# Kernel tuning notes

Measured on AMD Instinct MI355X. Metric: run time of the kernel, lower is better.

The kernel has to match this reference:

```python
import jax, jax.numpy as jnp
import numpy as np

E = 1024   # embed_dim
H = 16     # num_heads
D = E // H # head_dim
BS = 512   # block_size
G = 128    # global_len
B = 1
S = 8192


def setup_inputs() -> dict:
    key = jax.random.key(0)
    ks = jax.random.split(key, 7)
    w_scale = 0.02
    return {
        "token_hidden_states": jax.random.normal(ks[0], (B, S, E), jnp.float32),
        "global_hidden_states": jax.random.normal(ks[1], (B, G, E), jnp.float32),
        "attention_mask": jnp.zeros((B, S), jnp.float32),  # additive float mask
        "Wq": jax.random.normal(ks[2], (E, E), jnp.float32) * w_scale,
        "Wk": jax.random.normal(ks[3], (E, E), jnp.float32) * w_scale,
        "Wv": jax.random.normal(ks[4], (E, E), jnp.float32) * w_scale,
        "Wo": jax.random.normal(ks[5], (E, E), jnp.float32) * w_scale,
    }


def _shape(x):
    # [B, L, E] -> [B, H, L, D]
    b, l, _ = x.shape
    return x.reshape(b, l, H, D).transpose(0, 2, 1, 3)


def reference(token_hidden_states, global_hidden_states, attention_mask, Wq, Wk, Wv, Wo):
    b, s, _ = token_hidden_states.shape
    g = global_hidden_states.shape[1]
    n = s // BS  # num_blocks
    scaling = D ** -0.5

    local_q = _shape(token_hidden_states @ Wq * scaling)
    local_k = _shape(token_hidden_states @ Wk)
    local_v = _shape(token_hidden_states @ Wv)
    global_q = _shape(global_hidden_states @ Wq * scaling)
    global_k = _shape(global_hidden_states @ Wk)
    global_v = _shape(global_hidden_states @ Wv)

    # ---- global attention: global queries attend to [global + all local] keys
    k_cat = jnp.concatenate([global_k, local_k], axis=2)   # [B,H,G+S,D]
    v_cat = jnp.concatenate([global_v, local_v], axis=2)
    ext_mask = jnp.pad(attention_mask, ((0, 0), (g, 0)))    # [B,G+S]
    gw = jnp.einsum('bhgf,bhxf->bhgx', global_q, k_cat) + ext_mask[:, None, None, :]
    gp = jax.nn.softmax(gw, axis=-1)
    g_out = jnp.einsum('bhgx,bhxf->bhgf', gp, v_cat)        # [B,H,G,D]
    g_out = g_out.transpose(0, 2, 1, 3).reshape(b, g, E) @ Wo

    # ---- local attention: block-local + global keys
    bq = local_q.reshape(b, H, n, BS, D)
    bk = local_k.reshape(b, H, n, BS, D)
    bv = local_v.reshape(b, H, n, BS, D)
    ext_mask_l = jnp.pad(attention_mask.reshape(b, n, BS), ((0, 0), (0, 0), (g, 0)))  # [B,N,G+K]
    l2g = jnp.einsum('bhnkf,bhgf->bhnkg', bq, global_k)     # [B,H,N,K,G]
    l2l = jnp.einsum('bhnkf,bhnxf->bhnkx', bq, bk)          # [B,H,N,K,K]
    lw = jnp.concatenate([l2g, l2l], axis=-1) + ext_mask_l[:, None, :, None, :]
    lp = jax.nn.softmax(lw, axis=-1)
    l_out = (jnp.einsum('bhnkg,bhgf->bhnkf', lp[..., :g], global_v)
             + jnp.einsum('bhnkx,bhnxf->bhnkf', lp[..., g:], bv))  # [B,H,N,K,D]
    l_out = l_out.transpose(0, 2, 3, 1, 4).reshape(b, s, E) @ Wo

    return (l_out, g_out)
```

## Files before the change

kernel.cpp:

```cpp
#include <hip/hip_runtime.h>
#include <stdint.h>

#define S_LEN  8192
#define G_LEN  128
#define E_DIM  1024
#define H_NUM  16
#define BS_LEN 512
#define R_TOT  8320
#define KBLK   128
#define XBLK   1040
#define NSPL   10
#define SPLW   832

typedef _Float16 half8    __attribute__((ext_vector_type(8)));
typedef _Float16 half4    __attribute__((ext_vector_type(4)));
typedef float    floatx4  __attribute__((ext_vector_type(4)));
typedef float    floatx16 __attribute__((ext_vector_type(16)));

#define QSCALE 0.18033688011112042f

#define OFF_XP   0
#define OFF_AOP  0
#define OFF_WP   17039360
#define SZ_WP1   2097152
#define OFF_QP   25427968
#define OFF_KP   42467328
#define OFF_VP   59506688
#define OFF_FH   76546048
#define OFF_OG   76579328
#define OFF_LG   81822208

__device__ __forceinline__ floatx16 zero16() {
  floatx16 v;
#pragma unroll
  for (int i = 0; i < 16; ++i) v[i] = 0.0f;
  return v;
}
__device__ __forceinline__ floatx4 zero4() {
  floatx4 v;
#pragma unroll
  for (int i = 0; i < 4; ++i) v[i] = 0.0f;
  return v;
}

__device__ __forceinline__ void gl_lds16(const void* g, void* l) {
  __builtin_amdgcn_global_load_lds(
      (const __attribute__((address_space(1))) void*)g,
      (__attribute__((address_space(3))) void*)l, 16, 0, 0);
}

__device__ __forceinline__ int pk_f16x2(float a, float b) {
  return __builtin_bit_cast(int, __builtin_amdgcn_cvt_pkrtz(a, b));
}

__global__ __launch_bounds__(256) void prep_k(const float* __restrict__ tok,
                                              const float* __restrict__ glob,
                                              const float* __restrict__ Wq,
                                              const float* __restrict__ Wk,
                                              const float* __restrict__ Wv,
                                              const float* __restrict__ Wo,
                                              const float* __restrict__ mask,
                                              char* __restrict__ ws) {
  __shared__ __align__(16) _Float16 tile[64 * 132];
  const int bx  = blockIdx.x;
  const int tid = threadIdx.x;
  if (bx < 1040) {
    const int r0 = (bx >> 3) * 64;
    const int c0 = (bx & 7) * 128;
#pragma unroll
    for (int kk = 0; kk < 8; ++kk) {
      int f   = tid + kk * 256;
      int row = f >> 5;
      int c4  = (f & 31) * 4;
      int r   = r0 + row;
      const float* src = (r < G_LEN) ? glob + (size_t)r * E_DIM
                                     : tok + (size_t)(r - G_LEN) * E_DIM;
      float4 v = *(const float4*)&src[c0 + c4];
      half4 h;
      h[0] = (_Float16)v.x; h[1] = (_Float16)v.y; h[2] = (_Float16)v.z; h[3] = (_Float16)v.w;
      *(half4*)&tile[row * 132 + c4] = h;
    }
    __syncthreads();
    _Float16* Xp = (_Float16*)(ws + OFF_XP);
#pragma unroll
    for (int uu = 0; uu < 4; ++uu) {
      int u    = tid + uu * 256;
      int kb_l = u >> 6;
      int row  = u & 63;
      half4 a = *(const half4*)&tile[row * 132 + kb_l * 8];
      half4 b = *(const half4*)&tile[row * 132 + kb_l * 8 + 4];
      half8 o;
      o[0] = a[0]; o[1] = a[1]; o[2] = a[2]; o[3] = a[3];
      o[4] = b[0]; o[5] = b[1]; o[6] = b[2]; o[7] = b[3];
      int kb = (c0 >> 3) + kb_l;
      *(half8*)&Xp[((size_t)kb * R_TOT + r0 + row) * 8] = o;
    }
  } else {
    int t = (bx - 1040) * 256 + tid;
    const int NW = 4 * KBLK * 1024;
    if (t < NW) {
      int w   = t >> 17;
      int rem = t & 131071;
      int kb  = rem >> 10;
      int n   = rem & 1023;
      const float* W = (w == 0) ? Wq : (w == 1) ? Wk : (w == 2) ? Wv : Wo;
      half8 v;
#pragma unroll
      for (int j = 0; j < 8; ++j)
        v[j] = (_Float16)W[(size_t)(kb * 8 + j) * 1024 + n];
      *(half8*)(ws + OFF_WP + (size_t)w * SZ_WP1 + (size_t)(kb * 1024 + n) * 16) = v;
    } else {
      int t2 = t - NW;
      if (t2 < R_TOT) {
        _Float16* fh = (_Float16*)(ws + OFF_FH);
        float m = (t2 < G_LEN) ? 0.0f : mask[t2 - G_LEN];
        fh[t2] = (_Float16)__expf(m);
      }
    }
  }
}

__device__ __forceinline__ void gemm_tile(const _Float16* __restrict__ Ap,
                                          const _Float16* __restrict__ Bp,
                                          int m0, int n0, _Float16* lds,
                                          floatx4 acc[4][4]) {
  const int tid  = threadIdx.x;
  const int wave = tid >> 6;
  const int lane = tid & 63;
  const int quad = lane >> 4;
  const int l16  = lane & 15;
  _Float16* As = lds;
  _Float16* Bs = lds + 8 * 128 * 8;
  const int wm = (wave >> 1) * 64;
  const int wn = (wave & 1) * 64;
  for (int step = 0; step < 16; ++step) {
#pragma unroll
    for (int ui = 0; ui < 8; ++ui) {
      const int u   = wave * 8 + ui;
      const int isB = u >> 4;
      const int vv  = u & 15;
      const int kb  = vv >> 1;
      const int rh  = vv & 1;
      const _Float16* src =
          isB ? Bp + (size_t)((step * 8 + kb) * 1024 + n0 + rh * 64 + lane) * 8
              : Ap + (size_t)((step * 8 + kb) * R_TOT + m0 + rh * 64 + lane) * 8;
      _Float16* dst = (isB ? Bs : As) + (kb * 128 + rh * 64) * 8;
      gl_lds16(src, dst);
    }
    __syncthreads();
#pragma unroll
    for (int kk = 0; kk < 2; ++kk) {
      half8 af[4], bf[4];
#pragma unroll
      for (int mt = 0; mt < 4; ++mt)
        af[mt] = *(const half8*)(As + ((kk * 4 + quad) * 128 + wm + mt * 16 + l16) * 8);
#pragma unroll
      for (int nt = 0; nt < 4; ++nt)
        bf[nt] = *(const half8*)(Bs + ((kk * 4 + quad) * 128 + wn + nt * 16 + l16) * 8);
#pragma unroll
      for (int mt = 0; mt < 4; ++mt)
#pragma unroll
        for (int nt = 0; nt < 4; ++nt)
          acc[mt][nt] = __builtin_amdgcn_mfma_f32_16x16x32_f16(bf[nt], af[mt], acc[mt][nt], 0, 0, 0);
    }
    __syncthreads();
  }
}

__global__ __launch_bounds__(256) void qkv_gemm_k(char* __restrict__ ws) {
  __shared__ __align__(16) _Float16 lds[2 * 8 * 128 * 8];
  const int z  = blockIdx.x >> 3;
  const int n0 = (blockIdx.x & 7) * 128;
  const int m0 = blockIdx.y * 128;
  floatx4 acc[4][4];
#pragma unroll
  for (int a = 0; a < 4; ++a)
#pragma unroll
    for (int b = 0; b < 4; ++b) acc[a][b] = zero4();
  gemm_tile((const _Float16*)(ws + OFF_XP),
            (const _Float16*)(ws + OFF_WP + (size_t)z * SZ_WP1), m0, n0, lds, acc);

  const int lane = threadIdx.x & 63, wave = threadIdx.x >> 6;
  const int quad = lane >> 4, l16 = lane & 15;
  const int wm = (wave >> 1) * 64, wn = (wave & 1) * 64;
  if (z < 2) {
    _Float16* dst = (_Float16*)(ws + (z == 0 ? OFF_QP : OFF_KP));
    const float scale = (z == 0) ? QSCALE : 1.0f;
#pragma unroll
    for (int mt = 0; mt < 4; ++mt)
#pragma unroll
      for (int nt = 0; nt < 4; ++nt) {
        int m  = m0 + wm + mt * 16 + l16;
        int nb = n0 + wn + nt * 16 + quad * 4;
        half4 h;
#pragma unroll
        for (int r = 0; r < 4; ++r) h[r] = (_Float16)(acc[mt][nt][r] * scale);
        int db = (nb >> 6) * 8 + ((nb & 63) >> 3);
        *(half4*)&dst[((size_t)db * R_TOT + m) * 8 + (nb & 7)] = h;
      }
  } else {
    _Float16* dst = (_Float16*)(ws + OFF_VP);
    const _Float16* fh = (const _Float16*)(ws + OFF_FH);
#pragma unroll
    for (int mt = 0; mt < 4; ++mt) {
      int m = m0 + wm + mt * 16 + l16;
      float fhm = (float)fh[m];
#pragma unroll
      for (int nt = 0; nt < 4; ++nt) {
        int nl = n0 + wn + nt * 16 + quad * 4;
#pragma unroll
        for (int r = 0; r < 4; ++r) {
          int n = nl + r;
          dst[(((size_t)(n >> 6) * XBLK + (m >> 3)) * 64 + (n & 63)) * 8 + (m & 7)] =
              (_Float16)(acc[mt][nt][r] * fhm);
        }
      }
    }
  }
}

__device__ __forceinline__ void attn_core(const _Float16* __restrict__ Kph,
                                          const _Float16* __restrict__ Vph,
                                          const _Float16* __restrict__ fh,
                                          const half8 qa[4], int lane,
                                          int off, int seam, int nch,
                                          floatx16& o0, floatx16& o1, floatx16& lacc) {
  const int  half_ = lane >> 5;
  const int  c     = lane & 31;
  const bool hb    = half_ != 0;
  auto kbof = [&](int ci) { return ci * 32 + ((ci >= seam) ? off : 0); };

  half8 kf[4];
  const int kb0 = kbof(0);
#pragma unroll
  for (int ks = 0; ks < 4; ++ks)
    kf[ks] = *(const half8*)&Kph[(size_t)((ks * 2 + half_) * R_TOT + kb0 + c) * 8];
  floatx16 s = zero16();
#pragma unroll
  for (int ks = 0; ks < 4; ++ks)
    s = __builtin_amdgcn_mfma_f32_32x32x16_f16(kf[ks], qa[ks], s, 0, 0, 0);
  const int kb1 = kbof(nch > 1 ? 1 : 0);
#pragma unroll
  for (int ks = 0; ks < 4; ++ks)
    kf[ks] = *(const half8*)&Kph[(size_t)((ks * 2 + half_) * R_TOT + kb1 + c) * 8];

  for (int ci = 0; ci < nch; ++ci) {
    const int kb = kbof(ci);
    const int xb = kb >> 3;
    half8 vA0 = *(const half8*)&Vph[(size_t)((xb + half_) * 64 + c) * 8];
    half8 vA1 = *(const half8*)&Vph[(size_t)((xb + 2 + half_) * 64 + c) * 8];
    half8 vB0 = *(const half8*)&Vph[(size_t)((xb + half_) * 64 + 32 + c) * 8];
    half8 vB1 = *(const half8*)&Vph[(size_t)((xb + 2 + half_) * 64 + 32 + c) * 8];
    half8 f0 = *(const half8*)&fh[kb + half_ * 8];
    half8 f1 = *(const half8*)&fh[kb + 16 + half_ * 8];
    floatx16 sn = zero16();
#pragma unroll
    for (int ks = 0; ks < 4; ++ks)
      sn = __builtin_amdgcn_mfma_f32_32x32x16_f16(kf[ks], qa[ks], sn, 0, 0, 0);
    const int kbn = kbof(ci + 2 < nch ? ci + 2 : nch - 1);
#pragma unroll
    for (int ks = 0; ks < 4; ++ks)
      kf[ks] = *(const half8*)&Kph[(size_t)((ks * 2 + half_) * R_TOT + kbn + c) * 8];
    int pk[8];
#pragma unroll
    for (int i = 0; i < 8; ++i) {
      float e0 = __builtin_amdgcn_exp2f(s[2 * i]);
      float e1 = __builtin_amdgcn_exp2f(s[2 * i + 1]);
      pk[i] = pk_f16x2(e0, e1);
    }
    int sw[8];
#pragma unroll
    for (int i = 0; i < 8; ++i) sw[i] = __shfl_xor(pk[i], 32);
    int4 bi0, bi1;
    bi0.x = hb ? sw[2] : pk[0];  bi0.y = hb ? sw[3] : pk[1];
    bi0.z = hb ? pk[2] : sw[0];  bi0.w = hb ? pk[3] : sw[1];
    bi1.x = hb ? sw[6] : pk[4];  bi1.y = hb ? sw[7] : pk[5];
    bi1.z = hb ? pk[6] : sw[4];  bi1.w = hb ? pk[7] : sw[5];
    half8 b0 = __builtin_bit_cast(half8, bi0);
    half8 b1 = __builtin_bit_cast(half8, bi1);
    lacc = __builtin_amdgcn_mfma_f32_32x32x16_f16(f0, b0, lacc, 0, 0, 0);
    lacc = __builtin_amdgcn_mfma_f32_32x32x16_f16(f1, b1, lacc, 0, 0, 0);
    o0 = __builtin_amdgcn_mfma_f32_32x32x16_f16(vA0, b0, o0, 0, 0, 0);
    o0 = __builtin_amdgcn_mfma_f32_32x32x16_f16(vA1, b1, o0, 0, 0, 0);
    o1 = __builtin_amdgcn_mfma_f32_32x32x16_f16(vB0, b0, o1, 0, 0, 0);
    o1 = __builtin_amdgcn_mfma_f32_32x32x16_f16(vB1, b1, o1, 0, 0, 0);
    s = sn;
  }
}

__global__ __launch_bounds__(256) void attn_k(char* __restrict__ ws) {
  const int wave = threadIdx.x >> 6, lane = threadIdx.x & 63;
  const int bx = blockIdx.x;
  const _Float16* fh = (const _Float16*)(ws + OFF_FH);
  const int half_ = lane >> 5, c = lane & 31;
  if (bx < NSPL * H_NUM) {
    const int h = bx / NSPL, spl = bx % NSPL;
    const int qbase = wave * 32;
    const _Float16* Qph = (const _Float16*)(ws + OFF_QP) + (size_t)h * 8 * R_TOT * 8;
    const _Float16* Kph = (const _Float16*)(ws + OFF_KP) + (size_t)h * 8 * R_TOT * 8;
    const _Float16* Vph = (const _Float16*)(ws + OFF_VP) + (size_t)h * XBLK * 64 * 8;
    half8 qa[4];
#pragma unroll
    for (int ks = 0; ks < 4; ++ks)
      qa[ks] = *(const half8*)&Qph[(size_t)((ks * 2 + half_) * R_TOT + qbase + c) * 8];
    floatx16 o0 = zero16(), o1 = zero16(), l = zero16();
    attn_core(Kph, Vph, fh, qa, lane, spl * SPLW, 0, SPLW / 32, o0, o1, l);
    float* Og = (float*)(ws + OFF_OG);
    float* Lg = (float*)(ws + OFF_LG);
    const int q = qbase + c;
#pragma unroll
    for (int g = 0; g < 4; ++g) {
      float4 fa, fb;
      fa.x = o0[4 * g]; fa.y = o0[4 * g + 1]; fa.z = o0[4 * g + 2]; fa.w = o0[4 * g + 3];
      fb.x = o1[4 * g]; fb.y = o1[4 * g + 1]; fb.z = o1[4 * g + 2]; fb.w = o1[4 * g + 3];
      *(float4*)&Og[((size_t)(spl * H_NUM + h) * 128 + q) * 64 + 8 * g + 4 * half_] = fa;
      *(float4*)&Og[((size_t)(spl * H_NUM + h) * 128 + q) * 64 + 32 + 8 * g + 4 * half_] = fb;
    }
    if (half_ == 0) Lg[(spl * H_NUM + h) * 128 + q] = l[0];
  } else {
    const int t = bx - NSPL * H_NUM;
    const int h = t >> 6, blk = (t >> 2) & 15, qg = t & 3;
    const int qbase = G_LEN + blk * BS_LEN + qg * 128 + wave * 32;
    const _Float16* Qph = (const _Float16*)(ws + OFF_QP) + (size_t)h * 8 * R_TOT * 8;
    const _Float16* Kph = (const _Float16*)(ws + OFF_KP) + (size_t)h * 8 * R_TOT * 8;
    const _Float16* Vph = (const _Float16*)(ws + OFF_VP) + (size_t)h * XBLK * 64 * 8;
    half8 qa[4];
#pragma unroll
    for (int ks = 0; ks < 4; ++ks)
      qa[ks] = *(const half8*)&Qph[(size_t)((ks * 2 + half_) * R_TOT + qbase + c) * 8];
    floatx16 o0 = zero16(), o1 = zero16(), l = zero16();
    attn_core(Kph, Vph, fh, qa, lane, blk * BS_LEN, 4, 20, o0, o1, l);
    _Float16* AOp = (_Float16*)(ws + OFF_AOP);
    const float inv = 1.0f / l[0];
    const int m = qbase + c;
#pragma unroll
    for (int g = 0; g < 4; ++g) {
      half4 ha, hc;
#pragma unroll
      for (int i = 0; i < 4; ++i) {
        ha[i] = (_Float16)(o0[4 * g + i] * inv);
        hc[i] = (_Float16)(o1[4 * g + i] * inv);
      }
      *(half4*)&AOp[((size_t)(h * 8 + g) * R_TOT + m) * 8 + 4 * half_] = ha;
      *(half4*)&AOp[((size_t)(h * 8 + 4 + g) * R_TOT + m) * 8 + 4 * half_] = hc;
    }
  }
}

__global__ void combine_k(char* __restrict__ ws) {
  int idx = blockIdx.x * 256 + threadIdx.x;
  int h = idx >> 13, rem = idx & 8191, q = rem >> 6, d = rem & 63;
  const float* Og = (const float*)(ws + OFF_OG);
  const float* Lg = (const float*)(ws + OFF_LG);
  float o = 0.0f, l = 0.0f;
#pragma unroll
  for (int s = 0; s < NSPL; ++s) {
    o += Og[(size_t)((s * H_NUM + h) * 128 + q) * 64 + d];
    l += Lg[(s * H_NUM + h) * 128 + q];
  }
  int n = h * 64 + d;
  ((_Float16*)(ws + OFF_AOP))[((size_t)(n >> 3) * R_TOT + q) * 8 + (n & 7)] = (_Float16)(o / l);
}

__global__ __launch_bounds__(256) void out_gemm_k(char* __restrict__ ws, float* __restrict__ dout) {
  __shared__ __align__(16) _Float16 lds[2 * 8 * 128 * 8];
  const int m0 = blockIdx.y * 128;
  const int n0 = blockIdx.x * 128;
  floatx4 acc[4][4];
#pragma unroll
  for (int a = 0; a < 4; ++a)
#pragma unroll
    for (int b = 0; b < 4; ++b) acc[a][b] = zero4();
  gemm_tile((const _Float16*)(ws + OFF_AOP),
            (const _Float16*)(ws + OFF_WP + 3 * (size_t)SZ_WP1), m0, n0, lds, acc);
  const int lane = threadIdx.x & 63, wave = threadIdx.x >> 6;
  const int quad = lane >> 4, l16 = lane & 15;
  const int wm = (wave >> 1) * 64, wn = (wave & 1) * 64;
#pragma unroll
  for (int mt = 0; mt < 4; ++mt)
#pragma unroll
    for (int nt = 0; nt < 4; ++nt) {
      int m  = m0 + wm + mt * 16 + l16;
      int nb = n0 + wn + nt * 16 + quad * 4;
      float4 f4;
      f4.x = acc[mt][nt][0]; f4.y = acc[mt][nt][1];
      f4.z = acc[mt][nt][2]; f4.w = acc[mt][nt][3];
      float* p = (m < G_LEN) ? (dout + (size_t)S_LEN * E_DIM + (size_t)m * E_DIM + nb)
                             : (dout + (size_t)(m - G_LEN) * E_DIM + nb);
      *(float4*)p = f4;
    }
}

extern "C" void kernel_launch(void* const* d_in, const int* in_sizes, int n_in,
                              void* d_out, int out_size, void* d_ws, size_t ws_size,
                              hipStream_t stream) {
  const float* tok  = (const float*)d_in[0];
  const float* glob = (const float*)d_in[1];
  const float* mask = (const float*)d_in[2];
  const float* Wq   = (const float*)d_in[3];
  const float* Wk   = (const float*)d_in[4];
  const float* Wv   = (const float*)d_in[5];
  const float* Wo   = (const float*)d_in[6];
  char*  ws   = (char*)d_ws;
  float* dout = (float*)d_out;

  prep_k<<<dim3(1040 + 2081), dim3(256), 0, stream>>>(tok, glob, Wq, Wk, Wv, Wo, mask, ws);
  qkv_gemm_k<<<dim3(24, 65), dim3(256), 0, stream>>>(ws);
  attn_k<<<dim3(NSPL * H_NUM + 1024), dim3(256), 0, stream>>>(ws);
  combine_k<<<dim3(512), dim3(256), 0, stream>>>(ws);
  out_gemm_k<<<dim3(8, 65), dim3(256), 0, stream>>>(ws, dout);
}
```

Measured before the change: 254.3 us.

## Double-buffer B tiles in LDS and load A fragments directly to registers

Restructures the shared GEMM tile loop so the B operand is double-buffered in LDS and loaded for the next k-step while the current step computes. A fragments are no longer staged in LDS; each wave loads its own A fragments from global memory straight into registers, also one step ahead. This aims to hide global-load latency and halve LDS traffic, at the cost of more VGPRs (two sets of eight half8 A fragments), possible occupancy loss, and A rows being read redundantly by the two waves that share them.

```diff
diff --git a/kernel.cpp b/kernel.cpp
--- a/kernel.cpp
+++ b/kernel.cpp
@@ -120,6 +120,43 @@
   }
 }
 
+__device__ __forceinline__ void prefB(const _Float16* __restrict__ Bp, int n0, int step,
+                                      int wave, int lane, _Float16* Bs) {
+#pragma unroll
+  for (int ui = 0; ui < 4; ++ui) {
+    const int u  = wave * 4 + ui;
+    const int kb = u >> 1;
+    const int rh = u & 1;
+    gl_lds16(Bp + (size_t)((step * 8 + kb) * 1024 + n0 + rh * 64 + lane) * 8,
+             Bs + (kb * 128 + rh * 64) * 8);
+  }
+}
+__device__ __forceinline__ void prefA(const _Float16* __restrict__ Ap, int m0, int step,
+                                      int wm, int quad, int l16, half8 a[8]) {
+#pragma unroll
+  for (int kk = 0; kk < 2; ++kk)
+#pragma unroll
+    for (int mt = 0; mt < 4; ++mt)
+      a[kk * 4 + mt] = *(const half8*)&Ap[(size_t)((step * 8 + kk * 4 + quad) * R_TOT
+                                                   + m0 + wm + mt * 16 + l16) * 8];
+}
+__device__ __forceinline__ void compute_step(const half8 a[8], const _Float16* Bs,
+                                             int wn, int quad, int l16, floatx4 acc[4][4]) {
+#pragma unroll
+  for (int kk = 0; kk < 2; ++kk) {
+    half8 bf[4];
+#pragma unroll
+    for (int nt = 0; nt < 4; ++nt)
+      bf[nt] = *(const half8*)(Bs + ((kk * 4 + quad) * 128 + wn + nt * 16 + l16) * 8);
+#pragma unroll
+    for (int mt = 0; mt < 4; ++mt)
+#pragma unroll
+      for (int nt = 0; nt < 4; ++nt)
+        acc[mt][nt] = __builtin_amdgcn_mfma_f32_16x16x32_f16(bf[nt], a[kk * 4 + mt],
+                                                             acc[mt][nt], 0, 0, 0);
+  }
+}
+
 __device__ __forceinline__ void gemm_tile(const _Float16* __restrict__ Ap,
                                           const _Float16* __restrict__ Bp,
                                           int m0, int n0, _Float16* lds,
@@ -129,40 +166,26 @@
   const int lane = tid & 63;
   const int quad = lane >> 4;
   const int l16  = lane & 15;
-  _Float16* As = lds;
-  _Float16* Bs = lds + 8 * 128 * 8;
   const int wm = (wave >> 1) * 64;
   const int wn = (wave & 1) * 64;
-  for (int step = 0; step < 16; ++step) {
-#pragma unroll
-    for (int ui = 0; ui < 8; ++ui) {
-      const int u   = wave * 8 + ui;
-      const int isB = u >> 4;
-      const int vv  = u & 15;
-      const int kb  = vv >> 1;
-      const int rh  = vv & 1;
-      const _Float16* src =
-          isB ? Bp + (size_t)((step * 8 + kb) * 1024 + n0 + rh * 64 + lane) * 8
-              : Ap + (size_t)((step * 8 + kb) * R_TOT + m0 + rh * 64 + lane) * 8;
-      _Float16* dst = (isB ? Bs : As) + (kb * 128 + rh * 64) * 8;
-      gl_lds16(src, dst);
-    }
+  _Float16* Bs0 = lds;
+  _Float16* Bs1 = lds + 8 * 128 * 8;
+  half8 a_even[8], a_odd[8];
+
+  prefB(Bp, n0, 0, wave, lane, Bs0);
+  prefA(Ap, m0, 0, wm, quad, l16, a_even);
+  __syncthreads();
+  for (int s2 = 0; s2 < 8; ++s2) {
+    const int stepA = 2 * s2;
+    prefB(Bp, n0, stepA + 1, wave, lane, Bs1);
+    prefA(Ap, m0, stepA + 1, wm, quad, l16, a_odd);
+    compute_step(a_even, Bs0, wn, quad, l16, acc);
     __syncthreads();
-#pragma unroll
-    for (int kk = 0; kk < 2; ++kk) {
-      half8 af[4], bf[4];
-#pragma unroll
-      for (int mt = 0; mt < 4; ++mt)
-        af[mt] = *(const half8*)(As + ((kk * 4 + quad) * 128 + wm + mt * 16 + l16) * 8);
-#pragma unroll
-      for (int nt = 0; nt < 4; ++nt)
-        bf[nt] = *(const half8*)(Bs + ((kk * 4 + quad) * 128 + wn + nt * 16 + l16) * 8);
-#pragma unroll
-      for (int mt = 0; mt < 4; ++mt)
-#pragma unroll
-        for (int nt = 0; nt < 4; ++nt)
-          acc[mt][nt] = __builtin_amdgcn_mfma_f32_16x16x32_f16(bf[nt], af[mt], acc[mt][nt], 0, 0, 0);
-    }
+    if (s2 < 7) {
+      prefB(Bp, n0, stepA + 2, wave, lane, Bs0);
+      prefA(Ap, m0, stepA + 2, wm, quad, l16, a_even);
+    }
+    compute_step(a_odd, Bs1, wn, quad, l16, acc);
     __syncthreads();
   }
 }
```

Measured after the change: 256.9 us. Within noise of the previous version (+1.0%).

## Stage K/V chunks through double-buffered LDS shared by all waves

Applied to the files above, without the earlier changes.

Replaces per-wave global loads of K and V fragments in the attention loop with a cooperative double-buffered LDS staging scheme. Two waves load K and two load V for the next chunk via direct global-to-LDS copies, and all four waves then read fragments from shared memory. This removes the four-fold redundant global/L2 traffic, since each wave previously fetched the same K/V chunk. In exchange it adds a block-wide barrier per chunk and drops the register-level K prefetch and score pipelining.

```diff
diff --git a/kernel.cpp b/kernel.cpp
--- a/kernel.cpp
+++ b/kernel.cpp
@@ -219,48 +219,50 @@
   }
 }
 
-__device__ __forceinline__ void attn_core(const _Float16* __restrict__ Kph,
-                                          const _Float16* __restrict__ Vph,
-                                          const _Float16* __restrict__ fh,
-                                          const half8 qa[4], int lane,
-                                          int off, int seam, int nch,
-                                          floatx16& o0, floatx16& o1, floatx16& lacc) {
+__device__ __forceinline__ void attn_chunks_lds(const _Float16* __restrict__ Kph,
+                                                const _Float16* __restrict__ Vph,
+                                                const _Float16* __restrict__ fh,
+                                                const half8 qa[4], int wave, int lane,
+                                                int off, int seam, int nch,
+                                                _Float16 (* __restrict__ kv)[4096],
+                                                floatx16& o0, floatx16& o1, floatx16& lacc) {
   const int  half_ = lane >> 5;
   const int  c     = lane & 31;
   const bool hb    = half_ != 0;
   auto kbof = [&](int ci) { return ci * 32 + ((ci >= seam) ? off : 0); };
-
-  half8 kf[4];
-  const int kb0 = kbof(0);
-#pragma unroll
-  for (int ks = 0; ks < 4; ++ks)
-    kf[ks] = *(const half8*)&Kph[(size_t)((ks * 2 + half_) * R_TOT + kb0 + c) * 8];
-  floatx16 s = zero16();
-#pragma unroll
-  for (int ks = 0; ks < 4; ++ks)
-    s = __builtin_amdgcn_mfma_f32_32x32x16_f16(kf[ks], qa[ks], s, 0, 0, 0);
-  const int kb1 = kbof(nch > 1 ? 1 : 0);
-#pragma unroll
-  for (int ks = 0; ks < 4; ++ks)
-    kf[ks] = *(const half8*)&Kph[(size_t)((ks * 2 + half_) * R_TOT + kb1 + c) * 8];
-
+  auto stage = [&](int buf, int kb) {
+    if (wave < 2) {
+#pragma unroll
+      for (int j = 0; j < 2; ++j) {
+        const int u2  = wave * 2 + j;
+        const int db  = u2 * 2 + (lane >> 5);
+        const int key = lane & 31;
+        gl_lds16(&Kph[((size_t)db * R_TOT + kb + key) * 8], &kv[buf][u2 * 512]);
+      }
+    } else {
+#pragma unroll
+      for (int j = 0; j < 2; ++j) {
+        const int q4 = (wave - 2) * 2 + j;
+        gl_lds16(&Vph[(size_t)((kb >> 3) + q4) * 512 + (size_t)lane * 8],
+                 &kv[buf][2048 + q4 * 512]);
+      }
+    }
+  };
+
+  stage(0, kbof(0));
+  __syncthreads();
   for (int ci = 0; ci < nch; ++ci) {
+    const int cur = ci & 1;
+    if (ci + 1 < nch) stage(cur ^ 1, kbof(ci + 1));
+    const _Float16* Kb = kv[cur];
+    const _Float16* Vb = kv[cur] + 2048;
     const int kb = kbof(ci);
-    const int xb = kb >> 3;
-    half8 vA0 = *(const half8*)&Vph[(size_t)((xb + half_) * 64 + c) * 8];
-    half8 vA1 = *(const half8*)&Vph[(size_t)((xb + 2 + half_) * 64 + c) * 8];
-    half8 vB0 = *(const half8*)&Vph[(size_t)((xb + half_) * 64 + 32 + c) * 8];
-    half8 vB1 = *(const half8*)&Vph[(size_t)((xb + 2 + half_) * 64 + 32 + c) * 8];
-    half8 f0 = *(const half8*)&fh[kb + half_ * 8];
-    half8 f1 = *(const half8*)&fh[kb + 16 + half_ * 8];
-    floatx16 sn = zero16();
-#pragma unroll
-    for (int ks = 0; ks < 4; ++ks)
-      sn = __builtin_amdgcn_mfma_f32_32x32x16_f16(kf[ks], qa[ks], sn, 0, 0, 0);
-    const int kbn = kbof(ci + 2 < nch ? ci + 2 : nch - 1);
-#pragma unroll
-    for (int ks = 0; ks < 4; ++ks)
-      kf[ks] = *(const half8*)&Kph[(size_t)((ks * 2 + half_) * R_TOT + kbn + c) * 8];
+    floatx16 s = zero16();
+#pragma unroll
+    for (int ks = 0; ks < 4; ++ks) {
+      half8 kfr = *(const half8*)&Kb[((ks * 2 + half_) * 32 + c) * 8];
+      s = __builtin_amdgcn_mfma_f32_32x32x16_f16(kfr, qa[ks], s, 0, 0, 0);
+    }
     int pk[8];
 #pragma unroll
     for (int i = 0; i < 8; ++i) {
@@ -278,17 +280,24 @@
     bi1.z = hb ? pk[6] : sw[4];  bi1.w = hb ? pk[7] : sw[5];
     half8 b0 = __builtin_bit_cast(half8, bi0);
     half8 b1 = __builtin_bit_cast(half8, bi1);
+    half8 f0 = *(const half8*)&fh[kb + half_ * 8];
+    half8 f1 = *(const half8*)&fh[kb + 16 + half_ * 8];
     lacc = __builtin_amdgcn_mfma_f32_32x32x16_f16(f0, b0, lacc, 0, 0, 0);
     lacc = __builtin_amdgcn_mfma_f32_32x32x16_f16(f1, b1, lacc, 0, 0, 0);
+    half8 vA0 = *(const half8*)&Vb[(half_ * 64 + c) * 8];
+    half8 vA1 = *(const half8*)&Vb[((2 + half_) * 64 + c) * 8];
+    half8 vB0 = *(const half8*)&Vb[(half_ * 64 + 32 + c) * 8];
+    half8 vB1 = *(const half8*)&Vb[((2 + half_) * 64 + 32 + c) * 8];
     o0 = __builtin_amdgcn_mfma_f32_32x32x16_f16(vA0, b0, o0, 0, 0, 0);
     o0 = __builtin_amdgcn_mfma_f32_32x32x16_f16(vA1, b1, o0, 0, 0, 0);
     o1 = __builtin_amdgcn_mfma_f32_32x32x16_f16(vB0, b0, o1, 0, 0, 0);
     o1 = __builtin_amdgcn_mfma_f32_32x32x16_f16(vB1, b1, o1, 0, 0, 0);
-    s = sn;
+    __syncthreads();
   }
 }
 
 __global__ __launch_bounds__(256) void attn_k(char* __restrict__ ws) {
+  __shared__ __align__(16) _Float16 kv[2][4096];
   const int wave = threadIdx.x >> 6, lane = threadIdx.x & 63;
   const int bx = blockIdx.x;
   const _Float16* fh = (const _Float16*)(ws + OFF_FH);
@@ -304,7 +313,7 @@
     for (int ks = 0; ks < 4; ++ks)
       qa[ks] = *(const half8*)&Qph[(size_t)((ks * 2 + half_) * R_TOT + qbase + c) * 8];
     floatx16 o0 = zero16(), o1 = zero16(), l = zero16();
-    attn_core(Kph, Vph, fh, qa, lane, spl * SPLW, 0, SPLW / 32, o0, o1, l);
+    attn_chunks_lds(Kph, Vph, fh, qa, wave, lane, spl * SPLW, 0, SPLW / 32, kv, o0, o1, l);
     float* Og = (float*)(ws + OFF_OG);
     float* Lg = (float*)(ws + OFF_LG);
     const int q = qbase + c;
@@ -329,7 +338,7 @@
     for (int ks = 0; ks < 4; ++ks)
       qa[ks] = *(const half8*)&Qph[(size_t)((ks * 2 + half_) * R_TOT + qbase + c) * 8];
     floatx16 o0 = zero16(), o1 = zero16(), l = zero16();
-    attn_core(Kph, Vph, fh, qa, lane, blk * BS_LEN, 4, 20, o0, o1, l);
+    attn_chunks_lds(Kph, Vph, fh, qa, wave, lane, blk * BS_LEN, 4, 20, kv, o0, o1, l);
     _Float16* AOp = (_Float16*)(ws + OFF_AOP);
     const float inv = 1.0f / l[0];
     const int m = qbase + c;
```

Result: no change. 256.0 us (+0.7%).

## Process 64 queries per wave in attention to reuse K/V loads

Applied to the files above, without the earlier changes.

Each wave in the attention kernel now computes two 32-query tiles against the same K, V and mask fragments, which halves the K/V global loads per query. The grid shrinks from 1184 to 592 blocks, and global-query splits are remapped so each block covers two splits. The K prefetch depth also drops from two chunks ahead to one. The costs are roughly double the accumulator registers, which may lower occupancy, and less latency hiding for the K loads.

```diff
diff --git a/kernel.cpp b/kernel.cpp
--- a/kernel.cpp
+++ b/kernel.cpp
@@ -219,30 +219,22 @@
   }
 }
 
-__device__ __forceinline__ void attn_core(const _Float16* __restrict__ Kph,
-                                          const _Float16* __restrict__ Vph,
-                                          const _Float16* __restrict__ fh,
-                                          const half8 qa[4], int lane,
-                                          int off, int seam, int nch,
-                                          floatx16& o0, floatx16& o1, floatx16& lacc) {
+__device__ __forceinline__ void attn_core64(const _Float16* __restrict__ Kph,
+                                            const _Float16* __restrict__ Vph,
+                                            const _Float16* __restrict__ fh,
+                                            const half8 qaA[4], const half8 qaB[4],
+                                            int lane, int off, int seam, int nch,
+                                            floatx16& o0A, floatx16& o1A, floatx16& lA,
+                                            floatx16& o0B, floatx16& o1B, floatx16& lB) {
   const int  half_ = lane >> 5;
   const int  c     = lane & 31;
   const bool hb    = half_ != 0;
   auto kbof = [&](int ci) { return ci * 32 + ((ci >= seam) ? off : 0); };
 
   half8 kf[4];
-  const int kb0 = kbof(0);
 #pragma unroll
   for (int ks = 0; ks < 4; ++ks)
-    kf[ks] = *(const half8*)&Kph[(size_t)((ks * 2 + half_) * R_TOT + kb0 + c) * 8];
-  floatx16 s = zero16();
-#pragma unroll
-  for (int ks = 0; ks < 4; ++ks)
-    s = __builtin_amdgcn_mfma_f32_32x32x16_f16(kf[ks], qa[ks], s, 0, 0, 0);
-  const int kb1 = kbof(nch > 1 ? 1 : 0);
-#pragma unroll
-  for (int ks = 0; ks < 4; ++ks)
-    kf[ks] = *(const half8*)&Kph[(size_t)((ks * 2 + half_) * R_TOT + kb1 + c) * 8];
+    kf[ks] = *(const half8*)&Kph[(size_t)((ks * 2 + half_) * R_TOT + kbof(0) + c) * 8];
 
   for (int ci = 0; ci < nch; ++ci) {
     const int kb = kbof(ci);
@@ -253,38 +245,60 @@
     half8 vB1 = *(const half8*)&Vph[(size_t)((xb + 2 + half_) * 64 + 32 + c) * 8];
     half8 f0 = *(const half8*)&fh[kb + half_ * 8];
     half8 f1 = *(const half8*)&fh[kb + 16 + half_ * 8];
-    floatx16 sn = zero16();
-#pragma unroll
-    for (int ks = 0; ks < 4; ++ks)
-      sn = __builtin_amdgcn_mfma_f32_32x32x16_f16(kf[ks], qa[ks], sn, 0, 0, 0);
-    const int kbn = kbof(ci + 2 < nch ? ci + 2 : nch - 1);
+    floatx16 sA = zero16(), sB = zero16();
+#pragma unroll
+    for (int ks = 0; ks < 4; ++ks) {
+      sA = __builtin_amdgcn_mfma_f32_32x32x16_f16(kf[ks], qaA[ks], sA, 0, 0, 0);
+      sB = __builtin_amdgcn_mfma_f32_32x32x16_f16(kf[ks], qaB[ks], sB, 0, 0, 0);
+    }
+    const int kbn = kbof(ci + 1 < nch ? ci + 1 : ci);
 #pragma unroll
     for (int ks = 0; ks < 4; ++ks)
       kf[ks] = *(const half8*)&Kph[(size_t)((ks * 2 + half_) * R_TOT + kbn + c) * 8];
-    int pk[8];
-#pragma unroll
-    for (int i = 0; i < 8; ++i) {
-      float e0 = __builtin_amdgcn_exp2f(s[2 * i]);
-      float e1 = __builtin_amdgcn_exp2f(s[2 * i + 1]);
-      pk[i] = pk_f16x2(e0, e1);
-    }
-    int sw[8];
-#pragma unroll
-    for (int i = 0; i < 8; ++i) sw[i] = __shfl_xor(pk[i], 32);
-    int4 bi0, bi1;
-    bi0.x = hb ? sw[2] : pk[0];  bi0.y = hb ? sw[3] : pk[1];
-    bi0.z = hb ? pk[2] : sw[0];  bi0.w = hb ? pk[3] : sw[1];
-    bi1.x = hb ? sw[6] : pk[4];  bi1.y = hb ? sw[7] : pk[5];
-    bi1.z = hb ? pk[6] : sw[4];  bi1.w = hb ? pk[7] : sw[5];
-    half8 b0 = __builtin_bit_cast(half8, bi0);
-    half8 b1 = __builtin_bit_cast(half8, bi1);
-    lacc = __builtin_amdgcn_mfma_f32_32x32x16_f16(f0, b0, lacc, 0, 0, 0);
-    lacc = __builtin_amdgcn_mfma_f32_32x32x16_f16(f1, b1, lacc, 0, 0, 0);
-    o0 = __builtin_amdgcn_mfma_f32_32x32x16_f16(vA0, b0, o0, 0, 0, 0);
-    o0 = __builtin_amdgcn_mfma_f32_32x32x16_f16(vA1, b1, o0, 0, 0, 0);
-    o1 = __builtin_amdgcn_mfma_f32_32x32x16_f16(vB0, b0, o1, 0, 0, 0);
-    o1 = __builtin_amdgcn_mfma_f32_32x32x16_f16(vB1, b1, o1, 0, 0, 0);
-    s = sn;
+    {
+      int pk[8];
+#pragma unroll
+      for (int i = 0; i < 8; ++i)
+        pk[i] = pk_f16x2(__builtin_amdgcn_exp2f(sA[2 * i]), __builtin_amdgcn_exp2f(sA[2 * i + 1]));
+      int sw[8];
+#pragma unroll
+      for (int i = 0; i < 8; ++i) sw[i] = __shfl_xor(pk[i], 32);
+      int4 bi0, bi1;
+      bi0.x = hb ? sw[2] : pk[0];  bi0.y = hb ? sw[3] : pk[1];
+      bi0.z = hb ? pk[2] : sw[0];  bi0.w = hb ? pk[3] : sw[1];
+      bi1.x = hb ? sw[6] : pk[4];  bi1.y = hb ? sw[7] : pk[5];
+      bi1.z = hb ? pk[6] : sw[4];  bi1.w = hb ? pk[7] : sw[5];
+      half8 b0 = __builtin_bit_cast(half8, bi0);
+      half8 b1 = __builtin_bit_cast(half8, bi1);
+      lA  = __builtin_amdgcn_mfma_f32_32x32x16_f16(f0, b0, lA, 0, 0, 0);
+      lA  = __builtin_amdgcn_mfma_f32_32x32x16_f16(f1, b1, lA, 0, 0, 0);
+      o0A = __builtin_amdgcn_mfma_f32_32x32x16_f16(vA0, b0, o0A, 0, 0, 0);
+      o0A = __builtin_amdgcn_mfma_f32_32x32x16_f16(vA1, b1, o0A, 0, 0, 0);
+      o1A = __builtin_amdgcn_mfma_f32_32x32x16_f16(vB0, b0, o1A, 0, 0, 0);
+      o1A = __builtin_amdgcn_mfma_f32_32x32x16_f16(vB1, b1, o1A, 0, 0, 0);
+    }
+    {
+      int pk[8];
+#pragma unroll
+      for (int i = 0; i < 8; ++i)
+        pk[i] = pk_f16x2(__builtin_amdgcn_exp2f(sB[2 * i]), __builtin_amdgcn_exp2f(sB[2 * i + 1]));
+      int sw[8];
+#pragma unroll
+      for (int i = 0; i < 8; ++i) sw[i] = __shfl_xor(pk[i], 32);
+      int4 bi0, bi1;
+      bi0.x = hb ? sw[2] : pk[0];  bi0.y = hb ? sw[3] : pk[1];
+      bi0.z = hb ? pk[2] : sw[0];  bi0.w = hb ? pk[3] : sw[1];
+      bi1.x = hb ? sw[6] : pk[4];  bi1.y = hb ? sw[7] : pk[5];
+      bi1.z = hb ? pk[6] : sw[4];  bi1.w = hb ? pk[7] : sw[5];
+      half8 b0 = __builtin_bit_cast(half8, bi0);
+      half8 b1 = __builtin_bit_cast(half8, bi1);
+      lB  = __builtin_amdgcn_mfma_f32_32x32x16_f16(f0, b0, lB, 0, 0, 0);
+      lB  = __builtin_amdgcn_mfma_f32_32x32x16_f16(f1, b1, lB, 0, 0, 0);
+      o0B = __builtin_amdgcn_mfma_f32_32x32x16_f16(vA0, b0, o0B, 0, 0, 0);
+      o0B = __builtin_amdgcn_mfma_f32_32x32x16_f16(vA1, b1, o0B, 0, 0, 0);
+      o1B = __builtin_amdgcn_mfma_f32_32x32x16_f16(vB0, b0, o1B, 0, 0, 0);
+      o1B = __builtin_amdgcn_mfma_f32_32x32x16_f16(vB1, b1, o1B, 0, 0, 0);
+    }
   }
 }
 
@@ -293,56 +307,78 @@
   const int bx = blockIdx.x;
   const _Float16* fh = (const _Float16*)(ws + OFF_FH);
   const int half_ = lane >> 5, c = lane & 31;
-  if (bx < NSPL * H_NUM) {
-    const int h = bx / NSPL, spl = bx % NSPL;
-    const int qbase = wave * 32;
+  if (bx < 80) {
+    const int h = bx / 5, sp2 = bx % 5;
+    const int spl = sp2 * 2 + (wave >> 1);
+    const int qbase = (wave & 1) * 64;
     const _Float16* Qph = (const _Float16*)(ws + OFF_QP) + (size_t)h * 8 * R_TOT * 8;
     const _Float16* Kph = (const _Float16*)(ws + OFF_KP) + (size_t)h * 8 * R_TOT * 8;
     const _Float16* Vph = (const _Float16*)(ws + OFF_VP) + (size_t)h * XBLK * 64 * 8;
-    half8 qa[4];
-#pragma unroll
-    for (int ks = 0; ks < 4; ++ks)
-      qa[ks] = *(const half8*)&Qph[(size_t)((ks * 2 + half_) * R_TOT + qbase + c) * 8];
-    floatx16 o0 = zero16(), o1 = zero16(), l = zero16();
-    attn_core(Kph, Vph, fh, qa, lane, spl * SPLW, 0, SPLW / 32, o0, o1, l);
+    half8 qaA[4], qaB[4];
+#pragma unroll
+    for (int ks = 0; ks < 4; ++ks) {
+      qaA[ks] = *(const half8*)&Qph[(size_t)((ks * 2 + half_) * R_TOT + qbase + c) * 8];
+      qaB[ks] = *(const half8*)&Qph[(size_t)((ks * 2 + half_) * R_TOT + qbase + 32 + c) * 8];
+    }
+    floatx16 o0A = zero16(), o1A = zero16(), lA = zero16();
+    floatx16 o0B = zero16(), o1B = zero16(), lB = zero16();
+    attn_core64(Kph, Vph, fh, qaA, qaB, lane, spl * SPLW, 0, SPLW / 32,
+                o0A, o1A, lA, o0B, o1B, lB);
     float* Og = (float*)(ws + OFF_OG);
     float* Lg = (float*)(ws + OFF_LG);
-    const int q = qbase + c;
-#pragma unroll
-    for (int g = 0; g < 4; ++g) {
-      float4 fa, fb;
-      fa.x = o0[4 * g]; fa.y = o0[4 * g + 1]; fa.z = o0[4 * g + 2]; fa.w = o0[4 * g + 3];
-      fb.x = o1[4 * g]; fb.y = o1[4 * g + 1]; fb.z = o1[4 * g + 2]; fb.w = o1[4 * g + 3];
-      *(float4*)&Og[((size_t)(spl * H_NUM + h) * 128 + q) * 64 + 8 * g + 4 * half_] = fa;
-      *(float4*)&Og[((size_t)(spl * H_NUM + h) * 128 + q) * 64 + 32 + 8 * g + 4 * half_] = fb;
-    }
-    if (half_ == 0) Lg[(spl * H_NUM + h) * 128 + q] = l[0];
+#pragma unroll
+    for (int g2 = 0; g2 < 2; ++g2) {
+      const floatx16& o0 = g2 ? o0B : o0A;
+      const floatx16& o1 = g2 ? o1B : o1A;
+      const floatx16& l  = g2 ? lB  : lA;
+      const int q = qbase + g2 * 32 + c;
+#pragma unroll
+      for (int g = 0; g < 4; ++g) {
+        float4 fa, fb;
+        fa.x = o0[4 * g]; fa.y = o0[4 * g + 1]; fa.z = o0[4 * g + 2]; fa.w = o0[4 * g + 3];
+        fb.x = o1[4 * g]; fb.y = o1[4 * g + 1]; fb.z = o1[4 * g + 2]; fb.w = o1[4 * g + 3];
+        *(float4*)&Og[((size_t)(spl * H_NUM + h) * 128 + q) * 64 + 8 * g + 4 * half_] = fa;
+        *(float4*)&Og[((size_t)(spl * H_NUM + h) * 128 + q) * 64 + 32 + 8 * g + 4 * half_] = fb;
+      }
+      if (half_ == 0) Lg[(spl * H_NUM + h) * 128 + q] = l[0];
+    }
   } else {
-    const int t = bx - NSPL * H_NUM;
-    const int h = t >> 6, blk = (t >> 2) & 15, qg = t & 3;
-    const int qbase = G_LEN + blk * BS_LEN + qg * 128 + wave * 32;
+    const int item = bx - 80;
+    const int h = item >> 5, rem = item & 31;
+    const int blk = rem >> 1, qh = rem & 1;
+    const int qbase = G_LEN + blk * BS_LEN + qh * 256 + wave * 64;
     const _Float16* Qph = (const _Float16*)(ws + OFF_QP) + (size_t)h * 8 * R_TOT * 8;
     const _Float16* Kph = (const _Float16*)(ws + OFF_KP) + (size_t)h * 8 * R_TOT * 8;
     const _Float16* Vph = (const _Float16*)(ws + OFF_VP) + (size_t)h * XBLK * 64 * 8;
-    half8 qa[4];
-#pragma unroll
-    for (int ks = 0; ks < 4; ++ks)
-      qa[ks] = *(const half8*)&Qph[(size_t)((ks * 2 + half_) * R_TOT + qbase + c) * 8];
-    floatx16 o0 = zero16(), o1 = zero16(), l = zero16();
-    attn_core(Kph, Vph, fh, qa, lane, blk * BS_LEN, 4, 20, o0, o1, l);
+    half8 qaA[4], qaB[4];
+#pragma unroll
+    for (int ks = 0; ks < 4; ++ks) {
+      qaA[ks] = *(const half8*)&Qph[(size_t)((ks * 2 + half_) * R_TOT + qbase + c) * 8];
+      qaB[ks] = *(const half8*)&Qph[(size_t)((ks * 2 + half_) * R_TOT + qbase + 32 + c) * 8];
+    }
+    floatx16 o0A = zero16(), o1A = zero16(), lA = zero16();
+    floatx16 o0B = zero16(), o1B = zero16(), lB = zero16();
+    attn_core64(Kph, Vph, fh, qaA, qaB, lane, blk * BS_LEN, 4, 20,
+                o0A, o1A, lA, o0B, o1B, lB);
     _Float16* AOp = (_Float16*)(ws + OFF_AOP);
-    const float inv = 1.0f / l[0];
-    const int m = qbase + c;
-#pragma unroll
-    for (int g = 0; g < 4; ++g) {
-      half4 ha, hc;
-#pragma unroll
-      for (int i = 0; i < 4; ++i) {
-        ha[i] = (_Float16)(o0[4 * g + i] * inv);
-        hc[i] = (_Float16)(o1[4 * g + i] * inv);
+#pragma unroll
+    for (int g2 = 0; g2 < 2; ++g2) {
+      const floatx16& o0 = g2 ? o0B : o0A;
+      const floatx16& o1 = g2 ? o1B : o1A;
+      const floatx16& l  = g2 ? lB  : lA;
+      const float inv = 1.0f / l[0];
+      const int m = qbase + g2 * 32 + c;
+#pragma unroll
+      for (int g = 0; g < 4; ++g) {
+        half4 ha, hc;
+#pragma unroll
+        for (int i = 0; i < 4; ++i) {
+          ha[i] = (_Float16)(o0[4 * g + i] * inv);
+          hc[i] = (_Float16)(o1[4 * g + i] * inv);
+        }
+        *(half4*)&AOp[((size_t)(h * 8 + g) * R_TOT + m) * 8 + 4 * half_] = ha;
+        *(half4*)&AOp[((size_t)(h * 8 + 4 + g) * R_TOT + m) * 8 + 4 * half_] = hc;
       }
-      *(half4*)&AOp[((size_t)(h * 8 + g) * R_TOT + m) * 8 + 4 * half_] = ha;
-      *(half4*)&AOp[((size_t)(h * 8 + 4 + g) * R_TOT + m) * 8 + 4 * half_] = hc;
     }
   }
 }
@@ -406,7 +442,7 @@
 
   prep_k<<<dim3(1040 + 2081), dim3(256), 0, stream>>>(tok, glob, Wq, Wk, Wv, Wo, mask, ws);
   qkv_gemm_k<<<dim3(24, 65), dim3(256), 0, stream>>>(ws);
-  attn_k<<<dim3(NSPL * H_NUM + 1024), dim3(256), 0, stream>>>(ws);
+  attn_k<<<dim3(80 + 512), dim3(256), 0, stream>>>(ws);
   combine_k<<<dim3(512), dim3(256), 0, stream>>>(ws);
   out_gemm_k<<<dim3(8, 65), dim3(256), 0, stream>>>(ws, dout);
 }
```

Result: no change. 250.8 us (-1.4%).
